# Kernel optimization log

Measured on AMD Instinct MI355X. Metric: run time of the kernel, lower is better.

Reference implementation:

```python
import jax, jax.numpy as jnp
import numpy as np

D_MODEL = 2048
NUM_HEADS = 16
HEAD_DIM = D_MODEL // NUM_HEADS
ENTROPY_THRESHOLD = 0.01
B, T = 4, 2048


def setup_inputs() -> dict:
    key = jax.random.key(0)
    ks = jax.random.split(key, 10)
    s = 1.0 / np.sqrt(D_MODEL)
    inp = {
        "x": jax.random.normal(ks[0], (B, T, D_MODEL), dtype=jnp.float32),
        "mask": jnp.ones((B, T), dtype=jnp.int32),
        "Wq": jax.random.uniform(ks[1], (D_MODEL, D_MODEL), jnp.float32, -s, s),
        "bq": jax.random.uniform(ks[2], (D_MODEL,), jnp.float32, -s, s),
        "Wk": jax.random.uniform(ks[3], (D_MODEL, D_MODEL), jnp.float32, -s, s),
        "bk": jax.random.uniform(ks[4], (D_MODEL,), jnp.float32, -s, s),
        "Wv": jax.random.uniform(ks[5], (D_MODEL, D_MODEL), jnp.float32, -s, s),
        "bv": jax.random.uniform(ks[6], (D_MODEL,), jnp.float32, -s, s),
        "Wo": jax.random.uniform(ks[7], (D_MODEL, D_MODEL), jnp.float32, -s, s),
        "bo": jax.random.uniform(ks[8], (D_MODEL,), jnp.float32, -s, s),
    }
    return inp


def reference(x, mask, Wq, bq, Wk, bk, Wv, bv, Wo, bo):
    Bx, Tx, C = x.shape

    def heads(y):  # (B,T,C) -> (B,H,T,hd)
        return y.reshape(Bx, Tx, NUM_HEADS, HEAD_DIM).transpose(0, 2, 1, 3)

    q = heads(x @ Wq.T + bq)
    k = heads(x @ Wk.T + bk)
    v = heads(x @ Wv.T + bv)

    scores = jnp.einsum("bhqd,bhkd->bhqk", q, k) / np.sqrt(HEAD_DIM).astype(np.float32)
    scores = jnp.where(mask[:, None, None, :] == 0, -jnp.inf, scores)
    weights = jax.nn.softmax(scores, axis=-1)

    # entropy reduction (eval mode: conditional dropout is identity, so ent
    # does not alter the output, but we compute it faithfully)
    ent = -jnp.sum(weights * jnp.log(weights + 1e-9), axis=-1).mean()
    weights = jnp.where(ent < ENTROPY_THRESHOLD, weights, weights)  # dropout(p=0.1, training=False) == identity

    attended = jnp.einsum("bhqk,bhkd->bhqd", weights, v)
    attended = attended.transpose(0, 2, 1, 3).reshape(Bx, Tx, C)
    return attended @ Wo.T + bo
```

## Files before the change

### kernel.cpp

```cpp
#include <hip/hip_runtime.h>
#include <cstdint>
#include <cstddef>

#define D_MODEL 2048
#define T_SEQ   2048
#define N_BATCH 4
#define N_HEAD  16
#define HD      128
#define M_ROWS  (N_BATCH * T_SEQ)
#define N_QKV   (3 * D_MODEL)

typedef short          s8x  __attribute__((ext_vector_type(8)));
typedef float          f4x  __attribute__((ext_vector_type(4)));
typedef float          f4v  __attribute__((ext_vector_type(4)));
typedef unsigned short u16;
typedef u16            u16x8 __attribute__((ext_vector_type(8)));

__device__ __forceinline__ u16 f2bf(float f) {
    union { float f; unsigned u; } v; v.f = f;
    unsigned r = (v.u + 0x7FFFu + ((v.u >> 16) & 1u)) >> 16;
    return (u16)r;
}

__device__ __forceinline__ void glds16(const void* g, void* l) {
    __builtin_amdgcn_global_load_lds(
        (const __attribute__((address_space(1))) void*)g,
        (__attribute__((address_space(3))) void*)l, 16, 0, 0);
}

template<int CTRL>
__device__ __forceinline__ float dppror(float v) {
    int i = __builtin_bit_cast(int, v);
    int r = __builtin_amdgcn_update_dpp(i, i, CTRL, 0xf, 0xf, true);
    return __builtin_bit_cast(float, r);
}
__device__ __forceinline__ float rowmax16(float v) {
    v = fmaxf(v, dppror<0x128>(v));
    v = fmaxf(v, dppror<0x124>(v));
    v = fmaxf(v, dppror<0x122>(v));
    v = fmaxf(v, dppror<0x121>(v));
    return v;
}

__global__ void cvt_f32_bf16(const float* __restrict__ in, u16* __restrict__ out, int n8) {
    int i = blockIdx.x * blockDim.x + threadIdx.x;
    int stride = gridDim.x * blockDim.x;
    for (; i < n8; i += stride) {
        f4v a = reinterpret_cast<const f4v*>(in)[2 * i];
        f4v b = reinterpret_cast<const f4v*>(in)[2 * i + 1];
        u16x8 o;
        o[0] = f2bf(a[0]); o[1] = f2bf(a[1]); o[2] = f2bf(a[2]); o[3] = f2bf(a[3]);
        o[4] = f2bf(b[0]); o[5] = f2bf(b[1]); o[6] = f2bf(b[2]); o[7] = f2bf(b[3]);
        reinterpret_cast<u16x8*>(out)[i] = o;
    }
}

template<bool OUT_BF16>
__global__ __launch_bounds__(256)
void gemm_bt(const u16* __restrict__ A, const u16* __restrict__ B,
             const float* __restrict__ bias, void* __restrict__ C,
             int M, int N, int K, int nbn, float qscale, int qcols) {
    __shared__ u16 As[128 * 32];
    __shared__ u16 Bs[128 * 32];

    int nwg = gridDim.x;
    int wg  = blockIdx.x;
    int qx  = nwg >> 3;
    wg = (wg & 7) * qx + (wg >> 3);
    int bm = wg / nbn, bn = wg % nbn;

    int t   = threadIdx.x;
    int wid = t >> 6;
    int l15 = t & 15, l4 = (t >> 4) & 3;
    int wr  = wid >> 1, wc = wid & 1;

    f4x acc[4][4] = {};

    const u16* ga = A + (size_t)(bm * 128 + (t >> 2)) * K + (t & 3) * 8;
    const u16* gb = B + (size_t)(bn * 128 + (t >> 2)) * K + (t & 3) * 8;
    char* lA = (char*)As + wid * 1024;
    char* lB = (char*)Bs + wid * 1024;

    for (int k0 = 0; k0 < K; k0 += 32) {
        glds16(ga,              lA);
        glds16(ga + 64 * (size_t)K, lA + 4096);
        glds16(gb,              lB);
        glds16(gb + 64 * (size_t)K, lB + 4096);
        ga += 32; gb += 32;
        __syncthreads();

        s8x af[4], bfr[4];
        #pragma unroll
        for (int m = 0; m < 4; m++) {
            af[m]  = *reinterpret_cast<const s8x*>(As + (wr * 64 + m * 16 + l15) * 32 + l4 * 8);
            bfr[m] = *reinterpret_cast<const s8x*>(Bs + (wc * 64 + m * 16 + l15) * 32 + l4 * 8);
        }
        #pragma unroll
        for (int m = 0; m < 4; m++)
            #pragma unroll
            for (int n = 0; n < 4; n++)
                acc[m][n] = __builtin_amdgcn_mfma_f32_16x16x32_bf16(af[m], bfr[n], acc[m][n], 0, 0, 0);
        __syncthreads();
    }

    int row0 = bm * 128 + wr * 64;
    int col0 = bn * 128 + wc * 64;
    #pragma unroll
    for (int n = 0; n < 4; n++) {
        int col = col0 + n * 16 + l15;
        float bv = bias[col];
        float sc = (col < qcols) ? qscale : 1.0f;
        #pragma unroll
        for (int m = 0; m < 4; m++) {
            #pragma unroll
            for (int r = 0; r < 4; r++) {
                int row = row0 + m * 16 + l4 * 4 + r;
                float v = (acc[m][n][r] + bv) * sc;
                if (OUT_BF16) ((u16*)C)[(size_t)row * N + col]   = f2bf(v);
                else          ((float*)C)[(size_t)row * N + col] = v;
            }
        }
    }
}

__global__ __launch_bounds__(256, 2)
void attn(const u16* __restrict__ qkv, const int* __restrict__ mask,
          u16* __restrict__ att) {
    __shared__ u16  Vt[2][128 * 72];
    __shared__ u16  Pl[4][32 * 72];
    __shared__ float mbuf[2][64];

    int wg = blockIdx.x;
    int q8 = gridDim.x >> 3;
    wg = (wg & 7) * q8 + (wg >> 3);
    int bh = wg >> 4;
    int qb = wg & 15;
    int b  = bh >> 4, h = bh & 15;

    int t = threadIdx.x, wid = t >> 6;
    int lane = t & 63, l15 = lane & 15, l4 = lane >> 4;

    const size_t rs = N_QKV;
    const u16* qbase = qkv + (size_t)(b * T_SEQ) * rs;
    const u16* kbase = qbase + D_MODEL + h * HD;
    const u16* vbase = qbase + 2 * D_MODEL + h * HD;

    s8x qf[2][4];
    #pragma unroll
    for (int ms = 0; ms < 2; ms++)
        #pragma unroll
        for (int kk = 0; kk < 4; kk++) {
            int row = qb * 128 + wid * 32 + ms * 16 + l15;
            qf[ms][kk] = *reinterpret_cast<const s8x*>(
                qbase + (size_t)row * rs + h * HD + kk * 32 + l4 * 8);
        }

    f4x acc[2][8] = {};
    float mrun[2][4], lrun[2][4];
    #pragma unroll
    for (int ms = 0; ms < 2; ms++)
        #pragma unroll
        for (int r = 0; r < 4; r++) { mrun[ms][r] = -__builtin_inff(); lrun[ms][r] = 0.f; }

    int vp = t & 31;
    int vs = t >> 5;
    u16* Pw = Pl[wid];

    {
        s8x v0a = *reinterpret_cast<const s8x*>(vbase + (size_t)(2 * vp) * rs + vs * 16);
        s8x v0b = *reinterpret_cast<const s8x*>(vbase + (size_t)(2 * vp) * rs + vs * 16 + 8);
        s8x v1a = *reinterpret_cast<const s8x*>(vbase + (size_t)(2 * vp + 1) * rs + vs * 16);
        s8x v1b = *reinterpret_cast<const s8x*>(vbase + (size_t)(2 * vp + 1) * rs + vs * 16 + 8);
        if (t < 64) mbuf[0][t] = mask[b * T_SEQ + t] ? 0.f : -__builtin_inff();
        #pragma unroll
        for (int j = 0; j < 8; j++) {
            unsigned w0 = (u16)v0a[j] | ((unsigned)(u16)v1a[j] << 16);
            *reinterpret_cast<unsigned*>(&Vt[0][(vs * 16 + j) * 72 + 2 * vp]) = w0;
            unsigned w1 = (u16)v0b[j] | ((unsigned)(u16)v1b[j] << 16);
            *reinterpret_cast<unsigned*>(&Vt[0][(vs * 16 + 8 + j) * 72 + 2 * vp]) = w1;
        }
        __syncthreads();
    }

    for (int tt = 0; tt < T_SEQ / 64; tt++) {
        int kv0 = tt * 64;
        int cur = tt & 1, nxt = cur ^ 1;
        int kvn = kv0 + 64; if (kvn >= T_SEQ) kvn = 0;

        s8x v0a = *reinterpret_cast<const s8x*>(vbase + (size_t)(kvn + 2 * vp) * rs + vs * 16);
        s8x v0b = *reinterpret_cast<const s8x*>(vbase + (size_t)(kvn + 2 * vp) * rs + vs * 16 + 8);
        s8x v1a = *reinterpret_cast<const s8x*>(vbase + (size_t)(kvn + 2 * vp + 1) * rs + vs * 16);
        s8x v1b = *reinterpret_cast<const s8x*>(vbase + (size_t)(kvn + 2 * vp + 1) * rs + vs * 16 + 8);

        f4x sf[2][4] = {};
        #pragma unroll
        for (int t4 = 0; t4 < 4; t4++) {
            s8x kf[4];
            #pragma unroll
            for (int kk = 0; kk < 4; kk++)
                kf[kk] = *reinterpret_cast<const s8x*>(
                    kbase + (size_t)(kv0 + t4 * 16 + l15) * rs + kk * 32 + l4 * 8);
            #pragma unroll
            for (int ms = 0; ms < 2; ms++)
                #pragma unroll
                for (int kk = 0; kk < 4; kk++)
                    sf[ms][t4] = __builtin_amdgcn_mfma_f32_16x16x32_bf16(qf[ms][kk], kf[kk], sf[ms][t4], 0, 0, 0);
        }

        float mbv[4];
        #pragma unroll
        for (int t4 = 0; t4 < 4; t4++) mbv[t4] = mbuf[cur][t4 * 16 + l15];
        #pragma unroll
        for (int ms = 0; ms < 2; ms++)
            #pragma unroll
            for (int t4 = 0; t4 < 4; t4++)
                sf[ms][t4] += mbv[t4];

        #pragma unroll
        for (int ms = 0; ms < 2; ms++) {
            float mx[4];
            #pragma unroll
            for (int r = 0; r < 4; r++) {
                float a0 = fmaxf(fmaxf(sf[ms][0][r], sf[ms][1][r]),
                                 fmaxf(sf[ms][2][r], sf[ms][3][r]));
                mx[r] = rowmax16(a0);
            }
            f4x fv; float mc[4];
            #pragma unroll
            for (int r = 0; r < 4; r++) {
                float mn = fmaxf(mrun[ms][r], mx[r]);
                float f  = exp2f(mrun[ms][r] - mn);
                mrun[ms][r] = mn;
                lrun[ms][r] *= f;
                fv[r] = f;
                mc[r] = mn;
            }
            #pragma unroll
            for (int dt = 0; dt < 8; dt++) acc[ms][dt] *= fv;
            #pragma unroll
            for (int t4 = 0; t4 < 4; t4++) {
                #pragma unroll
                for (int r = 0; r < 4; r++) {
                    float p = exp2f(sf[ms][t4][r] - mc[r]);
                    lrun[ms][r] += p;
                    Pw[(ms * 16 + l4 * 4 + r) * 72 + t4 * 16 + l15] = f2bf(p);
                }
            }
        }
        asm volatile("" ::: "memory");

        s8x pa[2][2];
        #pragma unroll
        for (int ms = 0; ms < 2; ms++)
            #pragma unroll
            for (int ks = 0; ks < 2; ks++)
                pa[ms][ks] = *reinterpret_cast<const s8x*>(Pw + (ms * 16 + l15) * 72 + ks * 32 + l4 * 8);
        #pragma unroll
        for (int dt = 0; dt < 8; dt++) {
            s8x vbf[2];
            #pragma unroll
            for (int ks = 0; ks < 2; ks++)
                vbf[ks] = *reinterpret_cast<const s8x*>(&Vt[cur][(dt * 16 + l15) * 72 + ks * 32 + l4 * 8]);
            #pragma unroll
            for (int ms = 0; ms < 2; ms++)
                #pragma unroll
                for (int ks = 0; ks < 2; ks++)
                    acc[ms][dt] = __builtin_amdgcn_mfma_f32_16x16x32_bf16(pa[ms][ks], vbf[ks], acc[ms][dt], 0, 0, 0);
        }

        if (t < 64) mbuf[nxt][t] = mask[b * T_SEQ + kvn + t] ? 0.f : -__builtin_inff();
        #pragma unroll
        for (int j = 0; j < 8; j++) {
            unsigned w0 = (u16)v0a[j] | ((unsigned)(u16)v1a[j] << 16);
            *reinterpret_cast<unsigned*>(&Vt[nxt][(vs * 16 + j) * 72 + 2 * vp]) = w0;
            unsigned w1 = (u16)v0b[j] | ((unsigned)(u16)v1b[j] << 16);
            *reinterpret_cast<unsigned*>(&Vt[nxt][(vs * 16 + 8 + j) * 72 + 2 * vp]) = w1;
        }
        __syncthreads();
    }

    #pragma unroll
    for (int ms = 0; ms < 2; ms++) {
        f4x inv;
        #pragma unroll
        for (int r = 0; r < 4; r++) {
            float s = lrun[ms][r];
            #pragma unroll
            for (int sh = 1; sh <= 8; sh <<= 1) s += __shfl_xor(s, sh);
            inv[r] = 1.f / s;
        }
        #pragma unroll
        for (int dt = 0; dt < 8; dt++) {
            f4x o = acc[ms][dt] * inv;
            #pragma unroll
            for (int r = 0; r < 4; r++) {
                int row = qb * 128 + wid * 32 + ms * 16 + l4 * 4 + r;
                int col = h * HD + dt * 16 + l15;
                att[(size_t)(b * T_SEQ + row) * D_MODEL + col] = f2bf(o[r]);
            }
        }
    }
}

extern "C" void kernel_launch(void* const* d_in, const int* in_sizes, int n_in,
                              void* d_out, int out_size, void* d_ws, size_t ws_size,
                              hipStream_t stream) {
    (void)in_sizes; (void)n_in; (void)out_size; (void)ws_size;

    const float* x    = (const float*)d_in[0];
    const int*   mask = (const int*)d_in[1];
    const float* Wq   = (const float*)d_in[2];
    const float* bq   = (const float*)d_in[3];
    const float* Wk   = (const float*)d_in[4];
    const float* bk   = (const float*)d_in[5];
    const float* Wv   = (const float*)d_in[6];
    const float* bv   = (const float*)d_in[7];
    const float* Wo   = (const float*)d_in[8];
    const float* bo   = (const float*)d_in[9];
    float* out = (float*)d_out;

    char* ws = (char*)d_ws;
    u16*   xb   = (u16*)(ws);
    u16*   wqkv = (u16*)(ws + 33554432);
    u16*   wo   = (u16*)(ws + 58720256);
    float* bqkv = (float*)(ws + 67108864);
    u16*   qkvb = (u16*)(ws + 67133440);
    u16*   attb = (u16*)(ws + 167796736);

    cvt_f32_bf16<<<2048, 256, 0, stream>>>(x,  xb,               16777216 / 8);
    cvt_f32_bf16<<<1024, 256, 0, stream>>>(Wq, wqkv,              4194304 / 8);
    cvt_f32_bf16<<<1024, 256, 0, stream>>>(Wk, wqkv + 4194304,    4194304 / 8);
    cvt_f32_bf16<<<1024, 256, 0, stream>>>(Wv, wqkv + 8388608,    4194304 / 8);
    cvt_f32_bf16<<<1024, 256, 0, stream>>>(Wo, wo,                4194304 / 8);
    hipMemcpyAsync(bqkv,        bq, 2048 * 4, hipMemcpyDeviceToDevice, stream);
    hipMemcpyAsync(bqkv + 2048, bk, 2048 * 4, hipMemcpyDeviceToDevice, stream);
    hipMemcpyAsync(bqkv + 4096, bv, 2048 * 4, hipMemcpyDeviceToDevice, stream);

    const float cs = 0.08838834764831845f * 1.4426950408889634f;

    gemm_bt<true><<<64 * 48, 256, 0, stream>>>(xb, wqkv, bqkv, qkvb, M_ROWS, N_QKV, D_MODEL, 48, cs, D_MODEL);
    attn<<<1024, 256, 0, stream>>>(qkvb, mask, attb);
    gemm_bt<false><<<64 * 16, 256, 0, stream>>>(attb, wo, bo, out, M_ROWS, D_MODEL, D_MODEL, 16, 1.0f, 0);
}
```

Measured before the change: 880.9 us.

## Single-buffer swizzled V/P LDS tiles, raise occupancy, and skip unneeded softmax rescales

The attention kernel drops the double-buffered V tile and the padded 72-stride layout in favour of one XOR-swizzled 64-stride buffer for V and P. This shrinks LDS so launch bounds can ask for 4 blocks per CU instead of 2. Syncs are moved so that a single buffer is enough: one after QK^T, one before the next V write. The online-softmax rescale of the accumulator is skipped unless the row max grows by more than 8 (log2 units), which removes most per-tile multiplies. The costs are an extra barrier per iteration, a tighter register budget that could cause spills, and a stale max that can reach up to about 2^8, which should still be safe in fp32.

```diff
diff --git a/kernel.cpp b/kernel.cpp
--- a/kernel.cpp
+++ b/kernel.cpp
@@ -123,11 +123,11 @@
     }
 }
 
-__global__ __launch_bounds__(256, 2)
+__global__ __launch_bounds__(256, 4)
 void attn(const u16* __restrict__ qkv, const int* __restrict__ mask,
           u16* __restrict__ att) {
-    __shared__ u16  Vt[2][128 * 72];
-    __shared__ u16  Pl[4][32 * 72];
+    __shared__ u16  Vt[128 * 64];
+    __shared__ u16  Pl[4][32 * 64];
     __shared__ float mbuf[2][64];
 
     int wg = blockIdx.x;
@@ -174,12 +174,12 @@
         if (t < 64) mbuf[0][t] = mask[b * T_SEQ + t] ? 0.f : -__builtin_inff();
         #pragma unroll
         for (int j = 0; j < 8; j++) {
+            int r0 = vs * 16 + j, r1 = vs * 16 + 8 + j;
             unsigned w0 = (u16)v0a[j] | ((unsigned)(u16)v1a[j] << 16);
-            *reinterpret_cast<unsigned*>(&Vt[0][(vs * 16 + j) * 72 + 2 * vp]) = w0;
             unsigned w1 = (u16)v0b[j] | ((unsigned)(u16)v1b[j] << 16);
-            *reinterpret_cast<unsigned*>(&Vt[0][(vs * 16 + 8 + j) * 72 + 2 * vp]) = w1;
-        }
-        __syncthreads();
+            *reinterpret_cast<unsigned*>(&Vt[r0 * 64 + (((vp >> 2) ^ (r0 & 7)) << 3) + (vp & 3) * 2]) = w0;
+            *reinterpret_cast<unsigned*>(&Vt[r1 * 64 + (((vp >> 2) ^ (r1 & 7)) << 3) + (vp & 3) * 2]) = w1;
+        }
     }
 
     for (int tt = 0; tt < T_SEQ / 64; tt++) {
@@ -207,6 +207,8 @@
                     sf[ms][t4] = __builtin_amdgcn_mfma_f32_16x16x32_bf16(qf[ms][kk], kf[kk], sf[ms][t4], 0, 0, 0);
         }
 
+        __syncthreads();
+
         float mbv[4];
         #pragma unroll
         for (int t4 = 0; t4 < 4; t4++) mbv[t4] = mbuf[cur][t4 * 16 + l15];
@@ -225,25 +227,30 @@
                                  fmaxf(sf[ms][2][r], sf[ms][3][r]));
                 mx[r] = rowmax16(a0);
             }
-            f4x fv; float mc[4];
-            #pragma unroll
-            for (int r = 0; r < 4; r++) {
-                float mn = fmaxf(mrun[ms][r], mx[r]);
-                float f  = exp2f(mrun[ms][r] - mn);
-                mrun[ms][r] = mn;
-                lrun[ms][r] *= f;
-                fv[r] = f;
-                mc[r] = mn;
-            }
-            #pragma unroll
-            for (int dt = 0; dt < 8; dt++) acc[ms][dt] *= fv;
+            bool grow = false;
+            #pragma unroll
+            for (int r = 0; r < 4; r++) grow |= (mx[r] > mrun[ms][r] + 8.f);
+            if (__any(grow)) {
+                f4x fv;
+                #pragma unroll
+                for (int r = 0; r < 4; r++) {
+                    float mn = fmaxf(mrun[ms][r], mx[r]);
+                    fv[r] = exp2f(mrun[ms][r] - mn);
+                    mrun[ms][r] = mn;
+                    lrun[ms][r] *= fv[r];
+                }
+                #pragma unroll
+                for (int dt = 0; dt < 8; dt++) acc[ms][dt] *= fv;
+            }
             #pragma unroll
             for (int t4 = 0; t4 < 4; t4++) {
+                int pslot = (t4 << 1) + (l15 >> 3);
                 #pragma unroll
                 for (int r = 0; r < 4; r++) {
-                    float p = exp2f(sf[ms][t4][r] - mc[r]);
+                    float p = exp2f(sf[ms][t4][r] - mrun[ms][r]);
                     lrun[ms][r] += p;
-                    Pw[(ms * 16 + l4 * 4 + r) * 72 + t4 * 16 + l15] = f2bf(p);
+                    int prow = ms * 16 + l4 * 4 + r;
+                    Pw[prow * 64 + ((pslot ^ (prow & 7)) << 3) + (l15 & 7)] = f2bf(p);
                 }
             }
         }
@@ -253,14 +260,19 @@
         #pragma unroll
         for (int ms = 0; ms < 2; ms++)
             #pragma unroll
+            for (int ks = 0; ks < 2; ks++) {
+                int prow = ms * 16 + l15;
+                pa[ms][ks] = *reinterpret_cast<const s8x*>(
+                    Pw + prow * 64 + ((((ks << 2) + l4) ^ (prow & 7)) << 3));
+            }
+        #pragma unroll
+        for (int dt = 0; dt < 8; dt++) {
+            int vrow = dt * 16 + l15;
+            s8x vbf[2];
+            #pragma unroll
             for (int ks = 0; ks < 2; ks++)
-                pa[ms][ks] = *reinterpret_cast<const s8x*>(Pw + (ms * 16 + l15) * 72 + ks * 32 + l4 * 8);
-        #pragma unroll
-        for (int dt = 0; dt < 8; dt++) {
-            s8x vbf[2];
-            #pragma unroll
-            for (int ks = 0; ks < 2; ks++)
-                vbf[ks] = *reinterpret_cast<const s8x*>(&Vt[cur][(dt * 16 + l15) * 72 + ks * 32 + l4 * 8]);
+                vbf[ks] = *reinterpret_cast<const s8x*>(
+                    &Vt[vrow * 64 + ((((ks << 2) + l4) ^ (vrow & 7)) << 3)]);
             #pragma unroll
             for (int ms = 0; ms < 2; ms++)
                 #pragma unroll
@@ -268,15 +280,17 @@
                     acc[ms][dt] = __builtin_amdgcn_mfma_f32_16x16x32_bf16(pa[ms][ks], vbf[ks], acc[ms][dt], 0, 0, 0);
         }
 
+        __syncthreads();
+
         if (t < 64) mbuf[nxt][t] = mask[b * T_SEQ + kvn + t] ? 0.f : -__builtin_inff();
         #pragma unroll
         for (int j = 0; j < 8; j++) {
+            int r0 = vs * 16 + j, r1 = vs * 16 + 8 + j;
             unsigned w0 = (u16)v0a[j] | ((unsigned)(u16)v1a[j] << 16);
-            *reinterpret_cast<unsigned*>(&Vt[nxt][(vs * 16 + j) * 72 + 2 * vp]) = w0;
             unsigned w1 = (u16)v0b[j] | ((unsigned)(u16)v1b[j] << 16);
-            *reinterpret_cast<unsigned*>(&Vt[nxt][(vs * 16 + 8 + j) * 72 + 2 * vp]) = w1;
-        }
-        __syncthreads();
+            *reinterpret_cast<unsigned*>(&Vt[r0 * 64 + (((vp >> 2) ^ (r0 & 7)) << 3) + (vp & 3) * 2]) = w0;
+            *reinterpret_cast<unsigned*>(&Vt[r1 * 64 + (((vp >> 2) ^ (r1 & 7)) << 3) + (vp & 3) * 2]) = w1;
+        }
     }
 
     #pragma unroll
```

Measured after the change: 1.698 ms. 92.8% more time.
